# Kernel optimization log

Measured on AMD Instinct MI355X. Metric: run time of the kernel, lower is better.

The kernel has to match this reference:

```python
import jax, jax.numpy as jnp
import numpy as np

B, L, D, MAXL = 4, 2048, 1024, 4096

def setup_inputs() -> dict:
    key = jax.random.key(0)
    ks = jax.random.split(key, 7)
    x = jax.random.normal(ks[0], (B, L, D), dtype=jnp.float32)
    mask = jnp.ones((B, 1, L), dtype=jnp.int32)
    # kv_proj: Linear(D,D) -> ReLU -> Linear(D, 2D)
    s1 = 1.0 / np.sqrt(D)
    W1 = jax.random.uniform(ks[1], (D, D), minval=-s1, maxval=s1, dtype=jnp.float32)
    b1 = jax.random.uniform(ks[2], (D,), minval=-s1, maxval=s1, dtype=jnp.float32)
    W2 = jax.random.uniform(ks[3], (D, 2 * D), minval=-s1, maxval=s1, dtype=jnp.float32)
    b2 = jax.random.uniform(ks[4], (2 * D,), minval=-s1, maxval=s1, dtype=jnp.float32)
    D_to_L = jax.random.normal(ks[5], (D, MAXL), dtype=jnp.float32) * 0.01
    return {"x": x, "mask": mask, "W1": W1, "b1": b1, "W2": W2, "b2": b2, "D_to_L": D_to_L}

def reference(x, mask, W1, b1, W2, b2, D_to_L):
    Lcur = x.shape[1]
    h = jax.nn.relu(x @ W1 + b1)          # [B,L,D]
    kv = h @ W2 + b2                       # [B,L,2D]
    k, value = jnp.split(kv, 2, axis=-1)   # [B,L,D] each
    scores = jnp.einsum('bld,dk->blk', k, D_to_L[:, :Lcur])  # [B,L,L]
    scores = jnp.where(mask == 0, -jnp.inf, scores)
    attention = jax.nn.softmax(scores, axis=-1)
    output = attention @ value             # [B,L,D]
    return output, attention
```

## Files before the change

kernel.cpp:

```cpp
#include <hip/hip_runtime.h>
#include <cstdint>
#include <cstddef>

__device__ __forceinline__ uint16_t f2bf(float f) {
    union { float f; uint32_t i; } w; w.f = f;
    uint32_t x = w.i;
    uint32_t r = (x + 0x7FFFu + ((x >> 16) & 1u)) >> 16;
    return (uint16_t)r;
}

typedef __bf16 bf16x8 __attribute__((ext_vector_type(8)));
typedef float  f32x4  __attribute__((ext_vector_type(4)));

__device__ __forceinline__ void load_lds16(const void* gptr, void* lptr) {
    __builtin_amdgcn_global_load_lds(
        (__attribute__((address_space(1))) void*)gptr,
        (__attribute__((address_space(3))) void*)lptr,
        16, 0, 0);
}

template<int BN, int OUTFP32, int RELU>
__global__ __launch_bounds__(512, 2)
void gemm256(const uint16_t* __restrict__ A, const uint16_t* __restrict__ BT,
             const float* __restrict__ bias, void* __restrict__ Cv,
             int K, int lda, int ldb, int ldc,
             long long sB, int byShift)
{
    extern __shared__ uint16_t lds[];
    constexpr int SB  = (BN == 256) ? 2 : 1;
    constexpr int WN  = BN / 64;
    constexpr int MI  = 2 * WN;
    constexpr int SBE = BN * 32;

    const int g   = (int)blockIdx.x + (int)gridDim.x * (int)blockIdx.y;
    const int xcd = g & 7, ii = g >> 3;
    const int by  = xcd * 4 + (ii & 3);
    const int bx  = ii >> 2;
    const int gm0 = by * 256, gn0 = bx * BN;
    const int bz  = by >> byShift;
    BT += (long long)bz * sB;

    const int t    = threadIdx.x;
    const int w    = t >> 6, lane = t & 63;
    const int l15  = lane & 15, quad = lane >> 4;
    const int wr   = w / WN, wc = w % WN;

    const int cpr  = quad ^ ((l15 >> 1) & 3);
    const int arow = wr * (32 * WN) + l15;
    const int brow = wc * 64 + l15;

    const int r0 = t >> 2;
    const int qg = (t & 3) ^ ((t >> 3) & 3);
    const uint16_t* aS0 = A  + (size_t)(gm0 + r0) * lda + qg * 8;
    const uint16_t* aS1 = aS0 + (size_t)128 * lda;
    const uint16_t* bS0 = BT + (size_t)(gn0 + r0) * ldb + qg * 8;
    const uint16_t* bS1 = bS0 + (size_t)128 * ldb;
    const int ldw = w * 512;

#define SUBA(nb, kh) (lds + ((nb) * 2 + (kh)) * 8192)
#define SUBB(nb, kh) (lds + 32768 + ((nb) * 2 + (kh)) * SBE)
#define STAGE_A(nb, kh, k0s) do {                                               \
        load_lds16(aS0 + (k0s) + (kh) * 32, (void*)(SUBA(nb, kh) + ldw));       \
        load_lds16(aS1 + (k0s) + (kh) * 32, (void*)(SUBA(nb, kh) + 4096 + ldw));\
    } while (0)
#define STAGE_B(nb, kh, k0s) do {                                               \
        load_lds16(bS0 + (k0s) + (kh) * 32, (void*)(SUBB(nb, kh) + ldw));       \
        if constexpr (BN == 256)                                                \
            load_lds16(bS1 + (k0s) + (kh) * 32,                                 \
                       (void*)(SUBB(nb, kh) + 4096 + ldw));                     \
    } while (0)
#define VMW do {                                                                \
        if constexpr (SB == 2) asm volatile("s_waitcnt vmcnt(4)" ::: "memory"); \
        else                   asm volatile("s_waitcnt vmcnt(3)" ::: "memory"); \
    } while (0)
#define LGKM0 asm volatile("s_waitcnt lgkmcnt(0)" ::: "memory")
#define NOWAIT ((void)0)

    f32x4 acc[MI][4] = {};
    bf16x8 bF[4];

    STAGE_A(0, 0, 0); STAGE_B(0, 0, 0); STAGE_A(0, 1, 0); STAGE_B(0, 1, 0);
    VMW;
    __builtin_amdgcn_s_barrier();

    const int NT = K >> 6;
    for (int kt = 0; kt < NT; ++kt) {
        const int buf = kt & 1, nb = buf ^ 1;
        const int nk0 = (kt + 1 < NT) ? ((kt + 1) << 6) : 0;

        if constexpr (BN == 256) {
#define PHASE256(kh, mh, STAGE_STMT, VM_STMT)                                       \
            {                                                                       \
                const uint16_t* As_ = SUBA(buf, kh);                                \
                const uint16_t* Bs_ = SUBB(buf, kh);                                \
                bf16x8 aF[4];                                                       \
                _Pragma("unroll")                                                   \
                for (int i = 0; i < 4; i++)                                         \
                    aF[i] = *(const bf16x8*)(As_ + (arow + (mh) * 64 + i * 16) * 32 + cpr * 8); \
                if ((mh) == 0) {                                                    \
                    _Pragma("unroll")                                               \
                    for (int ni = 0; ni < 4; ni++)                                  \
                        bF[ni] = *(const bf16x8*)(Bs_ + (brow + ni * 16) * 32 + cpr * 8); \
                }                                                                   \
                STAGE_STMT;                                                         \
                __builtin_amdgcn_s_barrier();                                       \
                LGKM0;                                                              \
                __builtin_amdgcn_s_setprio(1);                                      \
                _Pragma("unroll")                                                   \
                for (int i = 0; i < 4; i++)                                         \
                    _Pragma("unroll")                                               \
                    for (int ni = 0; ni < 4; ni++)                                  \
                        acc[(mh) * 4 + i][ni] = __builtin_amdgcn_mfma_f32_16x16x32_bf16( \
                            aF[i], bF[ni], acc[(mh) * 4 + i][ni], 0, 0, 0);         \
                __builtin_amdgcn_s_setprio(0);                                      \
                VM_STMT;                                                            \
                __builtin_amdgcn_s_barrier();                                       \
            }
            PHASE256(0, 0, STAGE_A(nb, 0, nk0), NOWAIT)
            PHASE256(0, 1, STAGE_B(nb, 0, nk0), VMW)
            PHASE256(1, 0, STAGE_A(nb, 1, nk0), NOWAIT)
            PHASE256(1, 1, STAGE_B(nb, 1, nk0), VMW)
#undef PHASE256
        } else {
#define PHASE128(kh)                                                                \
            {                                                                       \
                const uint16_t* As_ = SUBA(buf, kh);                                \
                const uint16_t* Bs_ = SUBB(buf, kh);                                \
                bf16x8 aF[4], bG[4];                                                \
                _Pragma("unroll")                                                   \
                for (int i = 0; i < 4; i++)                                         \
                    aF[i] = *(const bf16x8*)(As_ + (arow + i * 16) * 32 + cpr * 8); \
                _Pragma("unroll")                                                   \
                for (int ni = 0; ni < 4; ni++)                                      \
                    bG[ni] = *(const bf16x8*)(Bs_ + (brow + ni * 16) * 32 + cpr * 8); \
                STAGE_A(nb, kh, nk0);                                               \
                STAGE_B(nb, kh, nk0);                                               \
                __builtin_amdgcn_s_barrier();                                       \
                LGKM0;                                                              \
                __builtin_amdgcn_s_setprio(1);                                      \
                _Pragma("unroll")                                                   \
                for (int i = 0; i < 4; i++)                                         \
                    _Pragma("unroll")                                               \
                    for (int ni = 0; ni < 4; ni++)                                  \
                        acc[i][ni] = __builtin_amdgcn_mfma_f32_16x16x32_bf16(       \
                            aF[i], bG[ni], acc[i][ni], 0, 0, 0);                    \
                __builtin_amdgcn_s_setprio(0);                                      \
                VMW;                                                                \
                __builtin_amdgcn_s_barrier();                                       \
            }
            PHASE128(0)
            PHASE128(1)
#undef PHASE128
        }
    }
    asm volatile("s_waitcnt vmcnt(0)" ::: "memory");

#pragma unroll
    for (int ni = 0; ni < 4; ni++) {
        const int gcol = gn0 + wc * 64 + ni * 16 + l15;
        const float bv = bias ? bias[gcol] : 0.0f;
#pragma unroll
        for (int mi = 0; mi < MI; mi++) {
#pragma unroll
            for (int r = 0; r < 4; r++) {
                const int grow = gm0 + wr * (32 * WN) + mi * 16 + quad * 4 + r;
                float v = acc[mi][ni][r] + bv;
                if (RELU) v = fmaxf(v, 0.0f);
                if (OUTFP32) ((float*)Cv)[(size_t)grow * ldc + gcol] = v;
                else         ((uint16_t*)Cv)[(size_t)grow * ldc + gcol] = f2bf(v);
            }
        }
    }
#undef SUBA
#undef SUBB
#undef STAGE_A
#undef STAGE_B
#undef VMW
#undef LGKM0
#undef NOWAIT
}

__global__ __launch_bounds__(256)
void cast_f32_bf16(const float* __restrict__ src, uint16_t* __restrict__ dst)
{
    const size_t i = ((size_t)blockIdx.x * 256 + threadIdx.x) * 8;
    float4 a = *(const float4*)(src + i);
    float4 b = *(const float4*)(src + i + 4);
    union { __bf16 h[8]; uint4 q; } u;
    u.h[0] = (__bf16)a.x; u.h[1] = (__bf16)a.y;
    u.h[2] = (__bf16)a.z; u.h[3] = (__bf16)a.w;
    u.h[4] = (__bf16)b.x; u.h[5] = (__bf16)b.y;
    u.h[6] = (__bf16)b.z; u.h[7] = (__bf16)b.w;
    *(uint4*)(dst + i) = u.q;
}

__global__ __launch_bounds__(256)
void transpose_f32_to_bf16(const float* __restrict__ src, uint16_t* __restrict__ dst,
                           int src_ld, int dst_ld)
{
    __shared__ uint16_t tile[64 * 65];
    const int k0 = blockIdx.y * 64, n0 = blockIdx.x * 64;
    const int t = threadIdx.x;
#pragma unroll
    for (int i = 0; i < 16; i++) {
        int idx = i * 256 + t;
        int r = idx >> 6, c = idx & 63;
        tile[c * 65 + r] = f2bf(src[(size_t)(k0 + r) * src_ld + n0 + c]);
    }
    __syncthreads();
#pragma unroll
    for (int i = 0; i < 16; i++) {
        int idx = i * 256 + t;
        int n = idx >> 6, k = idx & 63;
        dst[(size_t)(n0 + n) * dst_ld + k0 + k] = tile[n * 65 + k];
    }
}

__global__ __launch_bounds__(256)
void transpose_bf16(const uint16_t* __restrict__ src, uint16_t* __restrict__ dst,
                    int src_ld, int dst_ld, long long sS, long long sD)
{
    __shared__ uint16_t tile[64 * 65];
    src += (long long)blockIdx.z * sS;
    dst += (long long)blockIdx.z * sD;
    const int k0 = blockIdx.y * 64, n0 = blockIdx.x * 64;
    const int t = threadIdx.x;
#pragma unroll
    for (int i = 0; i < 16; i++) {
        int idx = i * 256 + t;
        int r = idx >> 6, c = idx & 63;
        tile[c * 65 + r] = src[(size_t)(k0 + r) * src_ld + n0 + c];
    }
    __syncthreads();
#pragma unroll
    for (int i = 0; i < 16; i++) {
        int idx = i * 256 + t;
        int n = idx >> 6, k = idx & 63;
        dst[(size_t)(n0 + n) * dst_ld + k0 + k] = tile[n * 65 + k];
    }
}

__global__ __launch_bounds__(256)
void softmax_rows_f32(float* __restrict__ S, uint16_t* __restrict__ Sbf,
                      const int* __restrict__ mask, int L)
{
    const int row = blockIdx.x;
    const int b = row >> 11;
    float* rp = S + (size_t)row * L;
    uint16_t* bp = Sbf + (size_t)row * L;
    const int* mrow = mask + (size_t)b * L;
    const int t = threadIdx.x;
    const int c0 = t * 8;

    float v[8];
    *(float4*)(v + 0) = *(const float4*)(rp + c0);
    *(float4*)(v + 4) = *(const float4*)(rp + c0 + 4);
    bool mk[8];
    float lmax = -1e30f;
#pragma unroll
    for (int j = 0; j < 8; j++) {
        mk[j] = (mrow[c0 + j] != 0);
        if (mk[j]) lmax = fmaxf(lmax, v[j]);
    }
#pragma unroll
    for (int off = 32; off > 0; off >>= 1)
        lmax = fmaxf(lmax, __shfl_xor(lmax, off, 64));

    __shared__ float redm[4];
    __shared__ float reds[4];
    const int w = t >> 6, lane = t & 63;
    if (lane == 0) redm[w] = lmax;
    __syncthreads();
    lmax = fmaxf(fmaxf(redm[0], redm[1]), fmaxf(redm[2], redm[3]));

    float e[8];
    float lsum = 0.f;
#pragma unroll
    for (int j = 0; j < 8; j++) {
        e[j] = mk[j] ? __expf(v[j] - lmax) : 0.0f;
        lsum += e[j];
    }
#pragma unroll
    for (int off = 32; off > 0; off >>= 1)
        lsum += __shfl_xor(lsum, off, 64);
    if (lane == 0) reds[w] = lsum;
    __syncthreads();
    lsum = reds[0] + reds[1] + reds[2] + reds[3];

    const float inv = 1.0f / lsum;
    uint16_t ub[8];
#pragma unroll
    for (int j = 0; j < 8; j++) {
        v[j] = e[j] * inv;
        ub[j] = f2bf(v[j]);
    }
    *(float4*)(rp + c0)     = *(const float4*)(v + 0);
    *(float4*)(rp + c0 + 4) = *(const float4*)(v + 4);
    *(uint4*)(bp + c0)      = *(const uint4*)ub;
}

extern "C" void kernel_launch(void* const* d_in, const int* in_sizes, int n_in,
                              void* d_out, int out_size, void* d_ws, size_t ws_size,
                              hipStream_t stream)
{
    const float* x    = (const float*)d_in[0];
    const int*   mask = (const int*)d_in[1];
    const float* W1   = (const float*)d_in[2];
    const float* b1   = (const float*)d_in[3];
    const float* W2   = (const float*)d_in[4];
    const float* b2   = (const float*)d_in[5];
    const float* D2L  = (const float*)d_in[6];

    const int Lr = 2048, D = 1024, M = 4 * Lr;
    float* outp = (float*)d_out;
    float* attn = outp + (size_t)M * D;

    uint16_t* W1T  = (uint16_t*)d_ws;
    uint16_t* W2T  = W1T + 1024 * 1024;
    uint16_t* D2LT = W2T + 2048 * 1024;
    uint16_t* hbuf = D2LT + 2048 * 1024;
    uint16_t* kv   = hbuf + (size_t)M * D;
    uint16_t* xbf  = kv + (size_t)M * 2048;
    uint16_t* vT   = hbuf;
    uint16_t* abf  = kv;

    dim3 blk(256);
    const dim3 g256(8, 32), b512(512);

    hipFuncSetAttribute(reinterpret_cast<const void*>(&gemm256<256, 0, 0>),
                        hipFuncAttributeMaxDynamicSharedMemorySize, 131072);
    hipFuncSetAttribute(reinterpret_cast<const void*>(&gemm256<256, 1, 0>),
                        hipFuncAttributeMaxDynamicSharedMemorySize, 131072);
    hipFuncSetAttribute(reinterpret_cast<const void*>(&gemm256<128, 0, 1>),
                        hipFuncAttributeMaxDynamicSharedMemorySize, 98304);
    hipFuncSetAttribute(reinterpret_cast<const void*>(&gemm256<128, 1, 0>),
                        hipFuncAttributeMaxDynamicSharedMemorySize, 98304);

    cast_f32_bf16<<<dim3(4096), blk, 0, stream>>>(x, xbf);

    transpose_f32_to_bf16<<<dim3(16, 16), blk, 0, stream>>>(W1,  W1T,  1024, 1024);
    transpose_f32_to_bf16<<<dim3(32, 16), blk, 0, stream>>>(W2,  W2T,  2048, 1024);
    transpose_f32_to_bf16<<<dim3(32, 16), blk, 0, stream>>>(D2L, D2LT, 4096, 1024);

    gemm256<128, 0, 1><<<g256, b512, 98304, stream>>>(xbf, W1T, b1, hbuf,
        1024, 1024, 1024, 1024, 0, 30);

    gemm256<256, 0, 0><<<g256, b512, 131072, stream>>>(hbuf, W2T, b2, kv,
        1024, 1024, 1024, 2048, 0, 30);

    transpose_bf16<<<dim3(16, 32, 4), blk, 0, stream>>>(kv + 1024, vT,
        2048, 2048, (long long)2048 * 2048, (long long)1024 * 2048);

    gemm256<256, 1, 0><<<g256, b512, 131072, stream>>>(kv, D2LT, nullptr, attn,
        1024, 2048, 1024, 2048, 0, 30);

    softmax_rows_f32<<<dim3(8192), blk, 0, stream>>>(attn, abf, mask, Lr);

    gemm256<128, 1, 0><<<g256, b512, 98304, stream>>>(abf, vT, nullptr, outp,
        2048, 2048, 2048, 1024, (long long)1024 * 2048, 3);
}
```

Measured before the change: 328.4 us.

## Fold key projection into score weights and compute V directly transposed

Uses associativity to precompute G = W2_k · D2L[:, :L] and a score bias b2_k · D2L, so scores become h·G plus that bias. This removes the 8192x1024 key projection and its bf16 write and read. The value projection is computed as W2_vᵀ · hᵀ with a row bias, writing vT directly and dropping the separate transpose kernel. It adds a small weight-by-weight GEMM, a serial bias-reduction kernel, a new grid-mapping parameter and reused workspace buffers, and it changes rounding because G is stored in bf16.

```diff
diff --git a/kernel.cpp b/kernel.cpp
--- a/kernel.cpp
+++ b/kernel.cpp
@@ -19,12 +19,12 @@
         16, 0, 0);
 }
 
-template<int BN, int OUTFP32, int RELU>
+template<int BN, int OUTFP32, int RELU, int ROWBIAS>
 __global__ __launch_bounds__(512, 2)
 void gemm256(const uint16_t* __restrict__ A, const uint16_t* __restrict__ BT,
              const float* __restrict__ bias, void* __restrict__ Cv,
              int K, int lda, int ldb, int ldc,
-             long long sB, int byShift)
+             long long sB, int byShift, int nbxShift)
 {
     extern __shared__ uint16_t lds[];
     constexpr int SB  = (BN == 256) ? 2 : 1;
@@ -34,8 +34,9 @@
 
     const int g   = (int)blockIdx.x + (int)gridDim.x * (int)blockIdx.y;
     const int xcd = g & 7, ii = g >> 3;
-    const int by  = xcd * 4 + (ii & 3);
-    const int bx  = ii >> 2;
+    const int q   = xcd * 32 + ii;
+    const int by  = q >> nbxShift;
+    const int bx  = q & ((1 << nbxShift) - 1);
     const int gm0 = by * 256, gn0 = bx * BN;
     const int bz  = by >> byShift;
     BT += (long long)bz * sB;
@@ -158,13 +159,13 @@
 #pragma unroll
     for (int ni = 0; ni < 4; ni++) {
         const int gcol = gn0 + wc * 64 + ni * 16 + l15;
-        const float bv = bias ? bias[gcol] : 0.0f;
+        const float bv = (!ROWBIAS && bias) ? bias[gcol] : 0.0f;
 #pragma unroll
         for (int mi = 0; mi < MI; mi++) {
 #pragma unroll
             for (int r = 0; r < 4; r++) {
                 const int grow = gm0 + wr * (32 * WN) + mi * 16 + quad * 4 + r;
-                float v = acc[mi][ni][r] + bv;
+                float v = acc[mi][ni][r] + (ROWBIAS ? bias[grow] : bv);
                 if (RELU) v = fmaxf(v, 0.0f);
                 if (OUTFP32) ((float*)Cv)[(size_t)grow * ldc + gcol] = v;
                 else         ((uint16_t*)Cv)[(size_t)grow * ldc + gcol] = f2bf(v);
@@ -178,6 +179,95 @@
 #undef VMW
 #undef LGKM0
 #undef NOWAIT
+}
+
+template<int AFP32, int OUTFP32, int RELU>
+__global__ __launch_bounds__(256, 3)
+void gemm_bt(const void* __restrict__ Av, const uint16_t* __restrict__ BT,
+             const float* __restrict__ bias, void* __restrict__ Cv,
+             int K, int lda, int ldb, int ldc,
+             long long sA, long long sB, long long sC)
+{
+    __shared__ uint16_t As[128 * 32];
+    __shared__ uint16_t Bs[128 * 32];
+
+    const int nx = (int)gridDim.x, ny = (int)gridDim.y, nz = (int)gridDim.z;
+    const int g   = (int)blockIdx.x + nx * ((int)blockIdx.y + ny * (int)blockIdx.z);
+    const int xcd = g & 7;
+    const int ii  = g >> 3;
+    const int xz  = 8 / nz;
+    const int bz  = xcd / xz;
+    const int sub = xcd % xz;
+    const int ypc = ny / xz;
+    const int by  = sub * ypc + ii % ypc;
+    const int bx  = ii / ypc;
+
+    const int t    = threadIdx.x;
+    const int lane = t & 63;
+    const int w    = t >> 6;
+    const int quad = lane >> 4;
+    const int l15  = lane & 15;
+    const int wr   = w >> 1;
+    const int wc   = w & 1;
+    const int gm0  = by * 128;
+    const int gn0  = bx * 128;
+
+    BT += (long long)bz * sB;
+
+    f32x4 acc[4][4] = {};
+
+    const int ch_r = lane >> 2;
+    const int ch_c = (lane & 3) * 8;
+
+    for (int k0 = 0; k0 < K; k0 += 32) {
+        __syncthreads();
+        {
+            int row = w * 16 + ch_r;
+            load_lds16(BT + (size_t)(gn0 + row) * ldb + k0 + ch_c, (void*)(Bs + w * 512));
+            load_lds16(BT + (size_t)(gn0 + row + 64) * ldb + k0 + ch_c, (void*)(Bs + (w + 4) * 512));
+        }
+        {
+            const uint16_t* A = (const uint16_t*)Av + (long long)bz * sA;
+            int row = w * 16 + ch_r;
+            load_lds16(A + (size_t)(gm0 + row) * lda + k0 + ch_c, (void*)(As + w * 512));
+            load_lds16(A + (size_t)(gm0 + row + 64) * lda + k0 + ch_c, (void*)(As + (w + 4) * 512));
+        }
+        __syncthreads();
+
+        bf16x8 af[4], bfr[4];
+#pragma unroll
+        for (int i = 0; i < 4; i++) {
+            af[i]  = *(const bf16x8*)(As + (wr * 64 + i * 16 + l15) * 32 + quad * 8);
+            bfr[i] = *(const bf16x8*)(Bs + (wc * 64 + i * 16 + l15) * 32 + quad * 8);
+        }
+#pragma unroll
+        for (int mi = 0; mi < 4; mi++)
+#pragma unroll
+            for (int ni = 0; ni < 4; ni++)
+                acc[mi][ni] = __builtin_amdgcn_mfma_f32_16x16x32_bf16(af[mi], bfr[ni], acc[mi][ni], 0, 0, 0);
+    }
+
+#pragma unroll
+    for (int ni = 0; ni < 4; ni++) {
+        const int gcol = gn0 + wc * 64 + ni * 16 + l15;
+        const float bv = bias ? bias[gcol] : 0.0f;
+#pragma unroll
+        for (int mi = 0; mi < 4; mi++) {
+#pragma unroll
+            for (int r = 0; r < 4; r++) {
+                const int grow = gm0 + wr * 64 + mi * 16 + quad * 4 + r;
+                float v = acc[mi][ni][r] + bv;
+                if (RELU) v = fmaxf(v, 0.0f);
+                if (OUTFP32) {
+                    float* C = (float*)Cv + (long long)bz * sC;
+                    C[(size_t)grow * ldc + gcol] = v;
+                } else {
+                    uint16_t* C = (uint16_t*)Cv + (long long)bz * sC;
+                    C[(size_t)grow * ldc + gcol] = f2bf(v);
+                }
+            }
+        }
+    }
 }
 
 __global__ __launch_bounds__(256)
@@ -217,27 +307,14 @@
 }
 
 __global__ __launch_bounds__(256)
-void transpose_bf16(const uint16_t* __restrict__ src, uint16_t* __restrict__ dst,
-                    int src_ld, int dst_ld, long long sS, long long sD)
-{
-    __shared__ uint16_t tile[64 * 65];
-    src += (long long)blockIdx.z * sS;
-    dst += (long long)blockIdx.z * sD;
-    const int k0 = blockIdx.y * 64, n0 = blockIdx.x * 64;
-    const int t = threadIdx.x;
-#pragma unroll
-    for (int i = 0; i < 16; i++) {
-        int idx = i * 256 + t;
-        int r = idx >> 6, c = idx & 63;
-        tile[c * 65 + r] = src[(size_t)(k0 + r) * src_ld + n0 + c];
-    }
-    __syncthreads();
-#pragma unroll
-    for (int i = 0; i < 16; i++) {
-        int idx = i * 256 + t;
-        int n = idx >> 6, k = idx & 63;
-        dst[(size_t)(n0 + n) * dst_ld + k0 + k] = tile[n * 65 + k];
-    }
+void score_bias(const float* __restrict__ b2, const float* __restrict__ D2L,
+                float* __restrict__ gb)
+{
+    const int n = blockIdx.x * 256 + threadIdx.x;
+    float s = 0.f;
+    for (int dd = 0; dd < 1024; ++dd)
+        s += b2[dd] * D2L[(size_t)dd * 4096 + n];
+    gb[n] = s;
 }
 
 __global__ __launch_bounds__(256)
@@ -316,46 +393,52 @@
     float* attn = outp + (size_t)M * D;
 
     uint16_t* W1T  = (uint16_t*)d_ws;
-    uint16_t* W2T  = W1T + 1024 * 1024;
-    uint16_t* D2LT = W2T + 2048 * 1024;
-    uint16_t* hbuf = D2LT + 2048 * 1024;
-    uint16_t* kv   = hbuf + (size_t)M * D;
-    uint16_t* xbf  = kv + (size_t)M * 2048;
-    uint16_t* vT   = hbuf;
-    uint16_t* abf  = kv;
+    uint16_t* W2T  = W1T + (size_t)1024 * 1024;
+    uint16_t* D2LT = W2T + (size_t)2048 * 1024;
+    uint16_t* hbuf = D2LT + (size_t)2048 * 1024;
+    uint16_t* vT   = hbuf + (size_t)M * D;
+    uint16_t* reg2 = vT + (size_t)1024 * 8192;
+    uint16_t* W2bf = reg2;
+    uint16_t* abf  = reg2;
+    uint16_t* reg3 = reg2 + (size_t)M * 2048;
+    uint16_t* xbf  = reg3;
+    uint16_t* GT   = reg3;
+    float*    gbuf = (float*)W1T;
 
     dim3 blk(256);
     const dim3 g256(8, 32), b512(512);
 
-    hipFuncSetAttribute(reinterpret_cast<const void*>(&gemm256<256, 0, 0>),
+    hipFuncSetAttribute(reinterpret_cast<const void*>(&gemm256<128, 0, 1, 0>),
+                        hipFuncAttributeMaxDynamicSharedMemorySize, 98304);
+    hipFuncSetAttribute(reinterpret_cast<const void*>(&gemm256<128, 0, 0, 1>),
+                        hipFuncAttributeMaxDynamicSharedMemorySize, 98304);
+    hipFuncSetAttribute(reinterpret_cast<const void*>(&gemm256<256, 1, 0, 0>),
                         hipFuncAttributeMaxDynamicSharedMemorySize, 131072);
-    hipFuncSetAttribute(reinterpret_cast<const void*>(&gemm256<256, 1, 0>),
-                        hipFuncAttributeMaxDynamicSharedMemorySize, 131072);
-    hipFuncSetAttribute(reinterpret_cast<const void*>(&gemm256<128, 0, 1>),
+    hipFuncSetAttribute(reinterpret_cast<const void*>(&gemm256<128, 1, 0, 0>),
                         hipFuncAttributeMaxDynamicSharedMemorySize, 98304);
-    hipFuncSetAttribute(reinterpret_cast<const void*>(&gemm256<128, 1, 0>),
-                        hipFuncAttributeMaxDynamicSharedMemorySize, 98304);
 
     cast_f32_bf16<<<dim3(4096), blk, 0, stream>>>(x, xbf);
-
+    cast_f32_bf16<<<dim3(1024), blk, 0, stream>>>(W2, W2bf);
     transpose_f32_to_bf16<<<dim3(16, 16), blk, 0, stream>>>(W1,  W1T,  1024, 1024);
     transpose_f32_to_bf16<<<dim3(32, 16), blk, 0, stream>>>(W2,  W2T,  2048, 1024);
     transpose_f32_to_bf16<<<dim3(32, 16), blk, 0, stream>>>(D2L, D2LT, 4096, 1024);
 
-    gemm256<128, 0, 1><<<g256, b512, 98304, stream>>>(xbf, W1T, b1, hbuf,
-        1024, 1024, 1024, 1024, 0, 30);
-
-    gemm256<256, 0, 0><<<g256, b512, 131072, stream>>>(hbuf, W2T, b2, kv,
-        1024, 1024, 1024, 2048, 0, 30);
-
-    transpose_bf16<<<dim3(16, 32, 4), blk, 0, stream>>>(kv + 1024, vT,
-        2048, 2048, (long long)2048 * 2048, (long long)1024 * 2048);
-
-    gemm256<256, 1, 0><<<g256, b512, 131072, stream>>>(kv, D2LT, nullptr, attn,
-        1024, 2048, 1024, 2048, 0, 30);
+    gemm256<128, 0, 1, 0><<<g256, b512, 98304, stream>>>(xbf, W1T, b1, hbuf,
+        1024, 1024, 1024, 1024, 0, 30, 3);
+
+    score_bias<<<dim3(8), blk, 0, stream>>>(b2, D2L, gbuf);
+
+    gemm_bt<0, 0, 0><<<dim3(8, 16, 1), blk, 0, stream>>>(D2LT, W2bf, nullptr, GT,
+        1024, 1024, 2048, 1024, 0, 0, 0);
+
+    gemm256<128, 0, 0, 1><<<g256, b512, 98304, stream>>>(W2T + (size_t)1024 * 1024,
+        hbuf, b2 + 1024, vT, 1024, 1024, 1024, 8192, 0, 30, 6);
+
+    gemm256<256, 1, 0, 0><<<g256, b512, 131072, stream>>>(hbuf, GT, gbuf, attn,
+        1024, 1024, 1024, 2048, 0, 30, 3);
 
     softmax_rows_f32<<<dim3(8192), blk, 0, stream>>>(attn, abf, mask, Lr);
 
-    gemm256<128, 1, 0><<<g256, b512, 98304, stream>>>(abf, vT, nullptr, outp,
-        2048, 2048, 2048, 1024, (long long)1024 * 2048, 3);
-}
+    gemm256<128, 1, 0, 0><<<g256, b512, 98304, stream>>>(abf, vT, nullptr, outp,
+        2048, 2048, 8192, 1024, 2048, 3, 3);
+}
```

Result: slower. 362.2 us (+10.3%).

## Fuse V transpose into KV GEMM epilogue and drop separate transpose kernel

Applied to the files above, without the earlier changes.

The second projection GEMM now writes K row-major into its own compact buffer. It writes V directly in transposed layout ([D][B*L]) from its epilogue, so the standalone bf16 transpose kernel and its extra read/write pass are removed. The final attention-times-V GEMM reads the transposed V with a batch offset instead of the old per-batch layout. Block-to-tile mapping is also generalised with a shift parameter that reorders tiles within each XCD. The transposed epilogue stores are 2-byte and strided across lanes, so they may coalesce poorly and offset the saved traffic.

```diff
diff --git a/kernel.cpp b/kernel.cpp
--- a/kernel.cpp
+++ b/kernel.cpp
@@ -19,12 +19,13 @@
         16, 0, 0);
 }
 
-template<int BN, int OUTFP32, int RELU>
+template<int BN, int OUTFP32, int RELU, int VSPLIT>
 __global__ __launch_bounds__(512, 2)
 void gemm256(const uint16_t* __restrict__ A, const uint16_t* __restrict__ BT,
              const float* __restrict__ bias, void* __restrict__ Cv,
+             uint16_t* __restrict__ C2,
              int K, int lda, int ldb, int ldc,
-             long long sB, int byShift)
+             long long sB, int byShift, int nbxShift)
 {
     extern __shared__ uint16_t lds[];
     constexpr int SB  = (BN == 256) ? 2 : 1;
@@ -34,8 +35,9 @@
 
     const int g   = (int)blockIdx.x + (int)gridDim.x * (int)blockIdx.y;
     const int xcd = g & 7, ii = g >> 3;
-    const int by  = xcd * 4 + (ii & 3);
-    const int bx  = ii >> 2;
+    const int q   = xcd * 32 + ii;
+    const int by  = q >> nbxShift;
+    const int bx  = q & ((1 << nbxShift) - 1);
     const int gm0 = by * 256, gn0 = bx * BN;
     const int bz  = by >> byShift;
     BT += (long long)bz * sB;
@@ -166,8 +168,16 @@
                 const int grow = gm0 + wr * (32 * WN) + mi * 16 + quad * 4 + r;
                 float v = acc[mi][ni][r] + bv;
                 if (RELU) v = fmaxf(v, 0.0f);
-                if (OUTFP32) ((float*)Cv)[(size_t)grow * ldc + gcol] = v;
-                else         ((uint16_t*)Cv)[(size_t)grow * ldc + gcol] = f2bf(v);
+                if (VSPLIT) {
+                    if (gcol < 1024)
+                        ((uint16_t*)Cv)[(size_t)grow * ldc + gcol] = f2bf(v);
+                    else
+                        C2[(size_t)(gcol - 1024) * 8192 + grow] = f2bf(v);
+                } else if (OUTFP32) {
+                    ((float*)Cv)[(size_t)grow * ldc + gcol] = v;
+                } else {
+                    ((uint16_t*)Cv)[(size_t)grow * ldc + gcol] = f2bf(v);
+                }
             }
         }
     }
@@ -217,30 +227,6 @@
 }
 
 __global__ __launch_bounds__(256)
-void transpose_bf16(const uint16_t* __restrict__ src, uint16_t* __restrict__ dst,
-                    int src_ld, int dst_ld, long long sS, long long sD)
-{
-    __shared__ uint16_t tile[64 * 65];
-    src += (long long)blockIdx.z * sS;
-    dst += (long long)blockIdx.z * sD;
-    const int k0 = blockIdx.y * 64, n0 = blockIdx.x * 64;
-    const int t = threadIdx.x;
-#pragma unroll
-    for (int i = 0; i < 16; i++) {
-        int idx = i * 256 + t;
-        int r = idx >> 6, c = idx & 63;
-        tile[c * 65 + r] = src[(size_t)(k0 + r) * src_ld + n0 + c];
-    }
-    __syncthreads();
-#pragma unroll
-    for (int i = 0; i < 16; i++) {
-        int idx = i * 256 + t;
-        int n = idx >> 6, k = idx & 63;
-        dst[(size_t)(n0 + n) * dst_ld + k0 + k] = tile[n * 65 + k];
-    }
-}
-
-__global__ __launch_bounds__(256)
 void softmax_rows_f32(float* __restrict__ S, uint16_t* __restrict__ Sbf,
                       const int* __restrict__ mask, int L)
 {
@@ -316,46 +302,42 @@
     float* attn = outp + (size_t)M * D;
 
     uint16_t* W1T  = (uint16_t*)d_ws;
-    uint16_t* W2T  = W1T + 1024 * 1024;
-    uint16_t* D2LT = W2T + 2048 * 1024;
-    uint16_t* hbuf = D2LT + 2048 * 1024;
-    uint16_t* kv   = hbuf + (size_t)M * D;
-    uint16_t* xbf  = kv + (size_t)M * 2048;
-    uint16_t* vT   = hbuf;
-    uint16_t* abf  = kv;
+    uint16_t* W2T  = W1T + (size_t)1024 * 1024;
+    uint16_t* D2LT = W2T + (size_t)2048 * 1024;
+    uint16_t* hbuf = D2LT + (size_t)2048 * 1024;
+    uint16_t* xbf  = hbuf + (size_t)M * D;
+    uint16_t* kbuf = xbf;
+    uint16_t* abf  = xbf;
+    uint16_t* vT   = xbf + (size_t)M * 2048;
 
     dim3 blk(256);
     const dim3 g256(8, 32), b512(512);
 
-    hipFuncSetAttribute(reinterpret_cast<const void*>(&gemm256<256, 0, 0>),
+    hipFuncSetAttribute(reinterpret_cast<const void*>(&gemm256<128, 0, 1, 0>),
+                        hipFuncAttributeMaxDynamicSharedMemorySize, 98304);
+    hipFuncSetAttribute(reinterpret_cast<const void*>(&gemm256<256, 0, 0, 1>),
                         hipFuncAttributeMaxDynamicSharedMemorySize, 131072);
-    hipFuncSetAttribute(reinterpret_cast<const void*>(&gemm256<256, 1, 0>),
+    hipFuncSetAttribute(reinterpret_cast<const void*>(&gemm256<256, 1, 0, 0>),
                         hipFuncAttributeMaxDynamicSharedMemorySize, 131072);
-    hipFuncSetAttribute(reinterpret_cast<const void*>(&gemm256<128, 0, 1>),
+    hipFuncSetAttribute(reinterpret_cast<const void*>(&gemm256<128, 1, 0, 0>),
                         hipFuncAttributeMaxDynamicSharedMemorySize, 98304);
-    hipFuncSetAttribute(reinterpret_cast<const void*>(&gemm256<128, 1, 0>),
-                        hipFuncAttributeMaxDynamicSharedMemorySize, 98304);
 
     cast_f32_bf16<<<dim3(4096), blk, 0, stream>>>(x, xbf);
-
     transpose_f32_to_bf16<<<dim3(16, 16), blk, 0, stream>>>(W1,  W1T,  1024, 1024);
     transpose_f32_to_bf16<<<dim3(32, 16), blk, 0, stream>>>(W2,  W2T,  2048, 1024);
     transpose_f32_to_bf16<<<dim3(32, 16), blk, 0, stream>>>(D2L, D2LT, 4096, 1024);
 
-    gemm256<128, 0, 1><<<g256, b512, 98304, stream>>>(xbf, W1T, b1, hbuf,
-        1024, 1024, 1024, 1024, 0, 30);
-
-    gemm256<256, 0, 0><<<g256, b512, 131072, stream>>>(hbuf, W2T, b2, kv,
-        1024, 1024, 1024, 2048, 0, 30);
-
-    transpose_bf16<<<dim3(16, 32, 4), blk, 0, stream>>>(kv + 1024, vT,
-        2048, 2048, (long long)2048 * 2048, (long long)1024 * 2048);
-
-    gemm256<256, 1, 0><<<g256, b512, 131072, stream>>>(kv, D2LT, nullptr, attn,
-        1024, 2048, 1024, 2048, 0, 30);
+    gemm256<128, 0, 1, 0><<<g256, b512, 98304, stream>>>(xbf, W1T, b1, hbuf, nullptr,
+        1024, 1024, 1024, 1024, 0, 30, 3);
+
+    gemm256<256, 0, 0, 1><<<g256, b512, 131072, stream>>>(hbuf, W2T, b2, kbuf, vT,
+        1024, 1024, 1024, 1024, 0, 30, 3);
+
+    gemm256<256, 1, 0, 0><<<g256, b512, 131072, stream>>>(kbuf, D2LT, nullptr, attn,
+        nullptr, 1024, 1024, 1024, 2048, 0, 30, 3);
 
     softmax_rows_f32<<<dim3(8192), blk, 0, stream>>>(attn, abf, mask, Lr);
 
-    gemm256<128, 1, 0><<<g256, b512, 98304, stream>>>(abf, vT, nullptr, outp,
-        2048, 2048, 2048, 1024, (long long)1024 * 2048, 3);
-}
+    gemm256<128, 1, 0, 0><<<g256, b512, 98304, stream>>>(abf, vT, nullptr, outp,
+        nullptr, 2048, 2048, 8192, 1024, 2048, 3, 3);
+}
```

After: 335.2 us. +2.1%, slower.
